# Kernel optimization log

Measured on AMD Instinct MI355X. Metric: run time of the kernel, lower is better.

The kernel has to match this reference:

```python
import jax, jax.numpy as jnp
import numpy as np

TOP_K = 8
NUM_EXPERTS = 64
N_TOKENS = 16384
N_EMBED = 4096
EPS = 1e-12  # F.normalize default eps


def setup_inputs() -> dict:
    key = jax.random.key(0)
    k_x, k_wr, k_br, k_wn, k_bn, k_noise = jax.random.split(key, 6)
    scale = 1.0 / np.sqrt(N_EMBED)
    return {
        "x": jax.random.normal(k_x, (N_TOKENS, N_EMBED), dtype=jnp.float32),
        "w_route": jax.random.normal(k_wr, (N_EMBED, NUM_EXPERTS), dtype=jnp.float32) * scale,
        "b_route": jax.random.normal(k_br, (NUM_EXPERTS,), dtype=jnp.float32) * scale,
        "w_noise": jax.random.normal(k_wn, (N_EMBED, NUM_EXPERTS), dtype=jnp.float32) * scale,
        "b_noise": jax.random.normal(k_bn, (NUM_EXPERTS,), dtype=jnp.float32) * scale,
        "noise": jax.random.normal(k_noise, (N_TOKENS, NUM_EXPERTS), dtype=jnp.float32),
    }


def _l1_normalize(v):
    return v / jnp.maximum(jnp.sum(jnp.abs(v)), EPS)


def reference(x, w_route, b_route, w_noise, b_noise, noise):
    # dual linear projections: [N, D] @ [D, E] -> [N, E]
    logits = x @ w_route + b_route
    noise_logits = x @ w_noise + b_noise
    noisy_logits = logits + noise * jax.nn.softplus(noise_logits)

    # top-k (sorted descending, matches torch.topk)
    top_vals, top_idx = jax.lax.top_k(noisy_logits, TOP_K)  # [N, K]
    rows = jnp.arange(noisy_logits.shape[0])[:, None]

    # scatter top-k logits into -inf, softmax -> sparse gate distribution
    sparse_logits = jnp.full_like(noisy_logits, -jnp.inf).at[rows, top_idx].set(top_vals)
    router_output = jax.nn.softmax(sparse_logits, axis=-1)  # [N, E]

    # aux loss (training path). Faithful to torch scatter semantics:
    # gates[n, top_idx[n, j]] = router_output[n, j] (first K columns of src).
    probs = jax.nn.softmax(noisy_logits, axis=-1)
    gates = jnp.zeros_like(probs).at[rows, top_idx].set(router_output[:, :TOP_K])
    probs_sum = probs.sum(0)                                  # [E]
    freq = (gates > 0).astype(jnp.float32).sum(0)             # [E]
    lsesq = jnp.sum(jax.nn.logsumexp(noisy_logits, axis=-1) ** 2)
    switchloss = NUM_EXPERTS * jnp.sum(_l1_normalize(probs_sum) * _l1_normalize(freq))
    zloss = lsesq / noisy_logits.shape[0]
    aux_loss = switchloss + 0.1 * zloss

    return router_output, top_idx, aux_loss
```

## Files before the change

kernel.cpp:

```cpp
#include <hip/hip_runtime.h>
#include <math.h>

#define NT 16384
#define NE 4096
#define NX 64
#define TK 8

#define BM 32
#define NBLK (NT / BM)
#define NSTEP 64

#define RO_SIZE (NT * NX)
#define TI_OFF  RO_SIZE
#define AUX_IDX (RO_SIZE + NT * TK)

#define MAXFLAG 8192
#define PSB_IDX 8256
#define FRB_IDX (PSB_IDX + NBLK * 64)
#define L2B_IDX (FRB_IDX + NBLK * 64)
#define WS_FLOATS (L2B_IDX + NBLK)
#define BPACK_OFF (((WS_FLOATS * 4) + 255) & ~255)
#define BPACK_USHORTS (128 * 4 * 2 * 128 * 8)
#define WS_NEED ((size_t)BPACK_OFF + (size_t)BPACK_USHORTS * 2)

#define DELTA_FP32 5e-5f
#define DELTA_BF16 2.5e-4f

typedef __attribute__((ext_vector_type(8))) short bf16x8_t;
typedef __attribute__((ext_vector_type(4))) float f32x4_t;

__device__ __forceinline__ float neginf() { return __int_as_float(0xff800000); }

__device__ __forceinline__ unsigned short bf16_trunc(float f) {
    return (unsigned short)(__float_as_uint(f) >> 16);
}
__device__ __forceinline__ unsigned short bf16_rtn(float f) {
    unsigned u = __float_as_uint(f);
    unsigned r = u + 0x7fffu + ((u >> 16) & 1u);
    return (unsigned short)(r >> 16);
}
__device__ __forceinline__ float bf16_to_f(unsigned short h) {
    return __uint_as_float(((unsigned)h) << 16);
}

__device__ __forceinline__ void split4(const float4& f,
                                       unsigned& h0, unsigned& h1,
                                       unsigned& l0, unsigned& l1) {
    unsigned u0 = __float_as_uint(f.x), u1 = __float_as_uint(f.y);
    unsigned u2 = __float_as_uint(f.z), u3 = __float_as_uint(f.w);
    h0 = __builtin_amdgcn_perm(u1, u0, 0x07060302u);
    h1 = __builtin_amdgcn_perm(u3, u2, 0x07060302u);
    float g0 = f.x - __uint_as_float(u0 & 0xffff0000u);
    float g1 = f.y - __uint_as_float(u1 & 0xffff0000u);
    float g2 = f.z - __uint_as_float(u2 & 0xffff0000u);
    float g3 = f.w - __uint_as_float(u3 & 0xffff0000u);
    l0 = __builtin_amdgcn_perm(__float_as_uint(g1), __float_as_uint(g0), 0x07060302u);
    l1 = __builtin_amdgcn_perm(__float_as_uint(g3), __float_as_uint(g2), 0x07060302u);
}

#define GLOAD16(GP, LP) __builtin_amdgcn_global_load_lds(                     \
    (const __attribute__((address_space(1))) void*)(GP),                      \
    (__attribute__((address_space(3))) void*)(LP), 16, 0, 0)

__global__ __launch_bounds__(512) void prep_w_kernel(
    const float* __restrict__ w_route, const float* __restrict__ w_noise,
    unsigned short* __restrict__ bp)
{
    const int kt = blockIdx.x;
    const int t = threadIdx.x;
    const int col = t & 127;
    const int kq = t >> 7;
    const float* src = (col < NX) ? (w_route + col) : (w_noise + (col - NX));
    const int kbase = kt * 32 + kq * 8;
    bf16x8_t h8, l8;
    #pragma unroll
    for (int i = 0; i < 8; ++i) {
        float v = src[(size_t)(kbase + i) * NX];
        unsigned short hh = bf16_trunc(v);
        h8[i] = (short)hh;
        l8[i] = (short)bf16_rtn(v - bf16_to_f(hh));
    }
    unsigned short* base = bp + ((size_t)((kt * 4 + kq) * 2) * 128 + col) * 8;
    *(bf16x8_t*)base = h8;
    *(bf16x8_t*)(base + 128 * 8) = l8;
}

__global__ __launch_bounds__(512, 4) void fused32_kernel(
    const float* __restrict__ x,
    const unsigned short* __restrict__ bp,
    const float* __restrict__ b_route, const float* __restrict__ b_noise,
    const float* __restrict__ noise,
    float* __restrict__ out,
    float* __restrict__ ps_blk, float* __restrict__ fr_blk,
    float* __restrict__ lse2_blk,
    int* __restrict__ flag_cnt, int* __restrict__ flag_list)
{
    __shared__ __align__(16) char ldsraw[81920];

    const int tid = threadIdx.x;
    const int wid = tid >> 6;
    const int lane = tid & 63;
    const int l15 = lane & 15;
    const int kq = lane >> 4;
    const int rg = wid >> 2;
    const int cgq = wid & 3;
    const int bm = blockIdx.x * BM;

    const int srow = tid >> 4;
    const int sq = tid & 15;
    const int skc = sq >> 1;
    const int shalf = sq & 1;
    const int srl = srow & 15;
    const int offA = srow * 256 + ((skc ^ srl) << 4) + shalf * 8;
    const float* sxa = x + (size_t)(bm + srow) * NE + sq * 4;

    char* ldsB = ldsraw + 16384;
    char* dB = ldsB + tid * 16;

    #define STAGE_B(BUF, ST) do {                                             \
        const unsigned short* sB_ = bp + (size_t)(ST) * 16384 + tid * 8;      \
        char* dB_ = dB + (BUF) * 32768;                                       \
        GLOAD16(sB_,         dB_);                                            \
        GLOAD16(sB_ + 4096,  dB_ + 8192);                                     \
        GLOAD16(sB_ + 8192,  dB_ + 16384);                                    \
        GLOAD16(sB_ + 12288, dB_ + 24576);                                    \
    } while (0)

    #define WRITE_A(BUF) do {                                                 \
        unsigned h0_, h1_, l0_, l1_;                                          \
        split4(rx, h0_, h1_, l0_, l1_);                                       \
        const int ob_ = (BUF) * 8192;                                         \
        *(int2*)(ldsraw + ob_ + offA)         = make_int2((int)h0_, (int)h1_);\
        *(int2*)(ldsraw + ob_ + (offA ^ 128)) = make_int2((int)l0_, (int)l1_);\
    } while (0)

    f32x4_t acc0 = (f32x4_t){0.f, 0.f, 0.f, 0.f};
    f32x4_t acc1 = (f32x4_t){0.f, 0.f, 0.f, 0.f};

    float4 rx = *(const float4*)(sxa);
    STAGE_B(0, 0);
    WRITE_A(0);
    __syncthreads();

    const char* aRow = ldsraw + (rg * 16 + l15) * 256;
    const int rl = l15;
    const int bBase = kq * 4096 + (cgq * 32 + l15) * 16;
    const int bLo   = bBase + 2048;

    for (int st = 0; st < NSTEP; ++st) {
        const int cur = st & 1;
        if (st + 1 < NSTEP) {
            rx = *(const float4*)(sxa + (st + 1) * 64);
            STAGE_B(cur ^ 1, st + 1);
        }

        const char* aB = aRow + cur * 8192;
        const char* bT = ldsB + cur * 32768;
        #pragma unroll
        for (int sub = 0; sub < 2; ++sub) {
            const int kcr = sub * 4 + kq;
            const int ch = (kcr ^ rl) << 4;
            bf16x8_t ah = *(const bf16x8_t*)(aB + ch);
            bf16x8_t al = *(const bf16x8_t*)(aB + (ch ^ 128));
            const char* bS = bT + sub * 16384;
            bf16x8_t bh0 = *(const bf16x8_t*)(bS + bBase);
            bf16x8_t bh1 = *(const bf16x8_t*)(bS + bBase + 256);
            bf16x8_t bl0 = *(const bf16x8_t*)(bS + bLo);
            bf16x8_t bl1 = *(const bf16x8_t*)(bS + bLo + 256);
            acc0 = __builtin_amdgcn_mfma_f32_16x16x32_bf16(ah, bh0, acc0, 0, 0, 0);
            acc1 = __builtin_amdgcn_mfma_f32_16x16x32_bf16(ah, bh1, acc1, 0, 0, 0);
            acc0 = __builtin_amdgcn_mfma_f32_16x16x32_bf16(al, bh0, acc0, 0, 0, 0);
            acc1 = __builtin_amdgcn_mfma_f32_16x16x32_bf16(al, bh1, acc1, 0, 0, 0);
            acc0 = __builtin_amdgcn_mfma_f32_16x16x32_bf16(ah, bl0, acc0, 0, 0, 0);
            acc1 = __builtin_amdgcn_mfma_f32_16x16x32_bf16(ah, bl1, acc1, 0, 0, 0);
        }

        if (st + 1 < NSTEP) WRITE_A(cur ^ 1);
        __syncthreads();
    }
    #undef STAGE_B
    #undef WRITE_A

    float (*part)[130] = (float (*)[130])ldsraw;
    #pragma unroll
    for (int j = 0; j < 4; ++j) {
        int tok = rg * 16 + (lane >> 4) * 4 + j;
        part[tok][cgq * 32 + l15]      = acc0[j];
        part[tok][cgq * 32 + 16 + l15] = acc1[j];
    }
    __syncthreads();

    const float br = b_route[lane];
    const float bnv = b_noise[lane];
    float ps_l = 0.f, fr_l = 0.f, l2_l = 0.f;

    for (int tt = 0; tt < 4; ++tt) {
        const int tok = wid * 4 + tt;
        const int gt  = bm + tok;
        float lr = part[tok][lane] + br;
        float ln = part[tok][64 + lane] + bnv;
        float nz = noise[(size_t)gt * NX + lane];
        float sp = fmaxf(ln, 0.f) + log1pf(expf(-fabsf(ln)));
        float v  = lr + nz * sp;

        float vv = v;
        float tv[9]; int ti[9];
        #pragma unroll
        for (int s = 0; s < 9; ++s) {
            float mv = vv; int mi = lane;
            #pragma unroll
            for (int off = 32; off > 0; off >>= 1) {
                float ov = __shfl_xor(mv, off);
                int   oi = __shfl_xor(mi, off);
                if (ov > mv || (ov == mv && oi < mi)) { mv = ov; mi = oi; }
            }
            tv[s] = mv; ti[s] = mi;
            if (lane == mi) vv = neginf();
        }

        float ming = 1e30f;
        #pragma unroll
        for (int s = 0; s < 8; ++s) ming = fminf(ming, tv[s] - tv[s + 1]);
        if (lane == 0 && ming < DELTA_BF16) {
            int p = atomicAdd(flag_cnt, 1);
            if (p < MAXFLAG) flag_list[p] = gt;
        }

        const float m0 = tv[0];
        float e8[8], s8 = 0.f;
        #pragma unroll
        for (int s = 0; s < 8; ++s) { e8[s] = expf(tv[s] - m0); s8 += e8[s]; }
        float r = 0.f;
        #pragma unroll
        for (int s = 0; s < 8; ++s) if (ti[s] == lane) r = e8[s] / s8;
        out[(size_t)gt * NX + lane] = r;
        if (lane < TK) out[TI_OFF + (size_t)gt * TK + lane] = (float)ti[lane];

        float p = expf(v - m0);
        float s64 = p;
        #pragma unroll
        for (int off = 32; off > 0; off >>= 1) s64 += __shfl_xor(s64, off);
        ps_l += p / s64;
        if (lane == 0) { float lse = m0 + logf(s64); l2_l += lse * lse; }

        unsigned tm8 = 0;
        #pragma unroll
        for (int s = 0; s < 8; ++s) if (ti[s] < TK) tm8 |= (1u << ti[s]);
        #pragma unroll
        for (int s = 0; s < 8; ++s)
            if (ti[s] == lane && ((tm8 >> s) & 1u)) fr_l += 1.f;
    }

    float* sps = (float*)(ldsraw + 20480);
    float* sfr = (float*)(ldsraw + 20480 + 2048);
    float* sl2 = (float*)(ldsraw + 20480 + 4096);
    sps[wid * 64 + lane] = ps_l;
    sfr[wid * 64 + lane] = fr_l;
    if (lane == 0) sl2[wid] = l2_l;
    __syncthreads();
    if (wid == 0) {
        float a = 0.f, b = 0.f;
        #pragma unroll
        for (int w = 0; w < 8; ++w) {
            a += sps[w * 64 + lane];
            b += sfr[w * 64 + lane];
        }
        ps_blk[(size_t)blockIdx.x * 64 + lane] = a;
        fr_blk[(size_t)blockIdx.x * 64 + lane] = b;
        if (lane == 0) {
            float z = 0.f;
            #pragma unroll
            for (int w = 0; w < 8; ++w) z += sl2[w];
            lse2_blk[blockIdx.x] = z;
        }
    }
}

#define FBM 64
#define FBN 128
#define FBK 32
#define XPITCH (FBM + 4)
__global__ __launch_bounds__(256) void fused_router_kernel(
    const float* __restrict__ x,
    const float* __restrict__ w_route, const float* __restrict__ b_route,
    const float* __restrict__ w_noise, const float* __restrict__ b_noise,
    const float* __restrict__ noise,
    float* __restrict__ out,
    float* __restrict__ ps_acc, float* __restrict__ fr_acc,
    float* __restrict__ lse2_acc,
    int* __restrict__ flag_cnt, int* __restrict__ flag_list)
{
    __shared__ float smem[FBM * FBN];
    float* xs  = smem;
    float* wst = smem + FBK * XPITCH;
    const int tid = threadIdx.x;
    const int block_m = blockIdx.x * FBM;
    const int row0 = (tid >> 5) * 8;
    const int col0 = (tid & 31) * 4;
    float acc[8][4];
    #pragma unroll
    for (int i = 0; i < 8; ++i)
        #pragma unroll
        for (int j = 0; j < 4; ++j) acc[i][j] = 0.f;
    float4 px[2], pw[4];
    {
        #pragma unroll
        for (int s = 0; s < 2; ++s) {
            int f = tid + s * 256, r = f >> 3, kqv = f & 7;
            px[s] = *reinterpret_cast<const float4*>(x + (size_t)(block_m + r) * NE + kqv * 4);
        }
        #pragma unroll
        for (int s = 0; s < 4; ++s) {
            int f = tid + s * 256, kk = f >> 5, c4 = (f & 31) * 4;
            const float* src = (c4 < NX) ? (w_route + (size_t)kk * NX + c4)
                                         : (w_noise + (size_t)kk * NX + (c4 - NX));
            pw[s] = *reinterpret_cast<const float4*>(src);
        }
    }
    for (int t = 0; t < NE / FBK; ++t) {
        __syncthreads();
        #pragma unroll
        for (int s = 0; s < 2; ++s) {
            int f = tid + s * 256, r = f >> 3, kqv = f & 7;
            xs[(kqv * 4 + 0) * XPITCH + r] = px[s].x;
            xs[(kqv * 4 + 1) * XPITCH + r] = px[s].y;
            xs[(kqv * 4 + 2) * XPITCH + r] = px[s].z;
            xs[(kqv * 4 + 3) * XPITCH + r] = px[s].w;
        }
        #pragma unroll
        for (int s = 0; s < 4; ++s) {
            int f = tid + s * 256, kk = f >> 5, c4 = (f & 31) * 4;
            *reinterpret_cast<float4*>(&wst[kk * FBN + c4]) = pw[s];
        }
        __syncthreads();
        if (t + 1 < NE / FBK) {
            const int k0 = (t + 1) * FBK;
            #pragma unroll
            for (int s = 0; s < 2; ++s) {
                int f = tid + s * 256, r = f >> 3, kqv = f & 7;
                px[s] = *reinterpret_cast<const float4*>(x + (size_t)(block_m + r) * NE + k0 + kqv * 4);
            }
            #pragma unroll
            for (int s = 0; s < 4; ++s) {
                int f = tid + s * 256, kk = f >> 5, c4 = (f & 31) * 4;
                const float* src = (c4 < NX) ? (w_route + (size_t)(k0 + kk) * NX + c4)
                                             : (w_noise + (size_t)(k0 + kk) * NX + (c4 - NX));
                pw[s] = *reinterpret_cast<const float4*>(src);
            }
        }
        #pragma unroll
        for (int k = 0; k < FBK; ++k) {
            float4 xa = *reinterpret_cast<const float4*>(&xs[k * XPITCH + row0]);
            float4 xb = *reinterpret_cast<const float4*>(&xs[k * XPITCH + row0 + 4]);
            float4 wv = *reinterpret_cast<const float4*>(&wst[k * FBN + col0]);
            float xf[8] = {xa.x, xa.y, xa.z, xa.w, xb.x, xb.y, xb.z, xb.w};
            float wf[4] = {wv.x, wv.y, wv.z, wv.w};
            #pragma unroll
            for (int i = 0; i < 8; ++i)
                #pragma unroll
                for (int j = 0; j < 4; ++j)
                    acc[i][j] = fmaf(xf[i], wf[j], acc[i][j]);
        }
    }
    __syncthreads();
    #pragma unroll
    for (int i = 0; i < 8; ++i) {
        float4 v = make_float4(acc[i][0], acc[i][1], acc[i][2], acc[i][3]);
        *reinterpret_cast<float4*>(&smem[(row0 + i) * FBN + col0]) = v;
    }
    __syncthreads();
    const int wave = tid >> 6;
    const int lane = tid & 63;
    const float br = b_route[lane];
    const float bnv = b_noise[lane];
    float ps_l = 0.f, fr_l = 0.f, l2_l = 0.f;
    for (int tt = 0; tt < FBM / 4; ++tt) {
        const int tok = wave * (FBM / 4) + tt;
        const int gt  = block_m + tok;
        float lr = smem[tok * FBN + lane] + br;
        float ln = smem[tok * FBN + NX + lane] + bnv;
        float nz = noise[(size_t)gt * NX + lane];
        float sp = fmaxf(ln, 0.f) + log1pf(expf(-fabsf(ln)));
        float v  = lr + nz * sp;
        float vv = v;
        float tv[9]; int ti[9];
        #pragma unroll
        for (int s = 0; s < 9; ++s) {
            float mv = vv; int mi = lane;
            #pragma unroll
            for (int off = 32; off > 0; off >>= 1) {
                float ov = __shfl_xor(mv, off);
                int   oi = __shfl_xor(mi, off);
                if (ov > mv || (ov == mv && oi < mi)) { mv = ov; mi = oi; }
            }
            tv[s] = mv; ti[s] = mi;
            if (lane == mi) vv = neginf();
        }
        float ming = 1e30f;
        #pragma unroll
        for (int s = 0; s < 8; ++s) ming = fminf(ming, tv[s] - tv[s + 1]);
        if (lane == 0 && ming < DELTA_FP32) {
            int p = atomicAdd(flag_cnt, 1);
            if (p < MAXFLAG) flag_list[p] = gt;
        }
        const float m0 = tv[0];
        float e8[8], s8 = 0.f;
        #pragma unroll
        for (int s = 0; s < 8; ++s) { e8[s] = expf(tv[s] - m0); s8 += e8[s]; }
        float r = 0.f;
        #pragma unroll
        for (int s = 0; s < 8; ++s) if (ti[s] == lane) r = e8[s] / s8;
        out[(size_t)gt * NX + lane] = r;
        if (lane < TK) out[TI_OFF + (size_t)gt * TK + lane] = (float)ti[lane];
        float p = expf(v - m0);
        float s64 = p;
        #pragma unroll
        for (int off = 32; off > 0; off >>= 1) s64 += __shfl_xor(s64, off);
        ps_l += p / s64;
        if (lane == 0) { float lse = m0 + logf(s64); l2_l += lse * lse; }
        unsigned tm8 = 0;
        #pragma unroll
        for (int s = 0; s < 8; ++s) if (ti[s] < TK) tm8 |= (1u << ti[s]);
        #pragma unroll
        for (int s = 0; s < 8; ++s)
            if (ti[s] == lane && ((tm8 >> s) & 1u)) fr_l += 1.f;
    }
    atomicAdd(&ps_acc[lane], ps_l);
    atomicAdd(&fr_acc[lane], fr_l);
    if (lane == 0) atomicAdd(lse2_acc, l2_l);
}

__global__ __launch_bounds__(256) void refine_kernel(
    const float* __restrict__ x, const float* __restrict__ w_route,
    const float* __restrict__ b_route, const float* __restrict__ w_noise,
    const float* __restrict__ b_noise, const float* __restrict__ noise,
    float* __restrict__ out, const int* __restrict__ flag_cnt,
    const int* __restrict__ flag_list)
{
    __shared__ double red[8][64];
    const int tid = threadIdx.x;
    const int lane = tid & 63, wq = tid >> 6;
    int nf = *flag_cnt; if (nf > MAXFLAG) nf = MAXFLAG;
    for (int fi = blockIdx.x; fi < nf; fi += gridDim.x) {
        const int gt = flag_list[fi];
        const float* xr = x + (size_t)gt * NE + wq * 1024;
        const float* wr = w_route + (size_t)wq * 1024 * NX;
        const float* wn = w_noise + (size_t)wq * 1024 * NX;
        double ar0 = 0, ar1 = 0, an0 = 0, an1 = 0;
        for (int k = 0; k < 1024; k += 2) {
            double x0 = xr[k], x1 = xr[k + 1];
            ar0 += x0 * (double)wr[(size_t)k * NX + lane];
            ar1 += x1 * (double)wr[(size_t)(k + 1) * NX + lane];
            an0 += x0 * (double)wn[(size_t)k * NX + lane];
            an1 += x1 * (double)wn[(size_t)(k + 1) * NX + lane];
        }
        red[wq * 2][lane]     = ar0 + ar1;
        red[wq * 2 + 1][lane] = an0 + an1;
        __syncthreads();
        if (tid < 64) {
            double lr = red[0][lane] + red[2][lane] + red[4][lane] + red[6][lane]
                      + (double)b_route[lane];
            double ln = red[1][lane] + red[3][lane] + red[5][lane] + red[7][lane]
                      + (double)b_noise[lane];
            double nz = (double)noise[(size_t)gt * NX + lane];
            double sp = (ln > 0.0) ? (ln + log1p(exp(-ln))) : log1p(exp(ln));
            double v  = lr + nz * sp;
            double vv = v;
            double tv[8]; int ti[8];
            #pragma unroll
            for (int s = 0; s < 8; ++s) {
                double mv = vv; int mi = lane;
                #pragma unroll
                for (int off = 32; off > 0; off >>= 1) {
                    double ov = __shfl_xor(mv, off);
                    int    oi = __shfl_xor(mi, off);
                    if (ov > mv || (ov == mv && oi < mi)) { mv = ov; mi = oi; }
                }
                tv[s] = mv; ti[s] = mi;
                if (lane == mi) vv = -1.0e300;
            }
            double m0 = tv[0], s8 = 0.0, e8[8];
            #pragma unroll
            for (int s = 0; s < 8; ++s) { e8[s] = exp(tv[s] - m0); s8 += e8[s]; }
            float r = 0.f;
            #pragma unroll
            for (int s = 0; s < 8; ++s) if (ti[s] == lane) r = (float)(e8[s] / s8);
            out[(size_t)gt * NX + lane] = r;
            if (lane < TK) out[TI_OFF + (size_t)gt * TK + lane] = (float)ti[lane];
        }
        __syncthreads();
    }
}

__global__ __launch_bounds__(512) void finalize_kernel(
    const float* __restrict__ ps_blk, const float* __restrict__ fr_blk,
    const float* __restrict__ lse2_blk, float* __restrict__ out)
{
    __shared__ float sps[8][64], sfr[8][64], sl2[512];
    const int t = threadIdx.x;
    const int e = t & 63, g = t >> 6;
    float a = 0.f, b = 0.f;
    for (int blk = g; blk < NBLK; blk += 8) {
        a += ps_blk[(size_t)blk * 64 + e];
        b += fr_blk[(size_t)blk * 64 + e];
    }
    sps[g][e] = a;
    sfr[g][e] = b;
    sl2[t] = lse2_blk[t];
    __syncthreads();
    if (t < 64) {
        float p = 0.f, f = 0.f;
        #pragma unroll
        for (int gg = 0; gg < 8; ++gg) { p += sps[gg][t]; f += sfr[gg][t]; }
        float z = 0.f;
        #pragma unroll
        for (int i = 0; i < 8; ++i) z += sl2[t * 8 + i];
        float sp = p, sf = f, sz = z;
        #pragma unroll
        for (int off = 32; off > 0; off >>= 1) {
            sp += __shfl_xor(sp, off);
            sf += __shfl_xor(sf, off);
            sz += __shfl_xor(sz, off);
        }
        float d = (p / fmaxf(sp, 1e-12f)) * (f / fmaxf(sf, 1e-12f));
        #pragma unroll
        for (int off = 32; off > 0; off >>= 1) d += __shfl_xor(d, off);
        if (t == 0)
            out[AUX_IDX] = 64.f * d + 0.1f * (sz / (float)NT);
    }
}

extern "C" void kernel_launch(void* const* d_in, const int* in_sizes, int n_in,
                              void* d_out, int out_size, void* d_ws, size_t ws_size,
                              hipStream_t stream) {
    const float* x       = (const float*)d_in[0];
    const float* w_route = (const float*)d_in[1];
    const float* b_route = (const float*)d_in[2];
    const float* w_noise = (const float*)d_in[3];
    const float* b_noise = (const float*)d_in[4];
    const float* noise   = (const float*)d_in[5];
    float* out = (float*)d_out;

    float* wsf = (float*)d_ws;
    int* flag_cnt  = (int*)wsf;
    int* flag_list = (int*)(wsf + 1);
    float* ps_blk   = wsf + PSB_IDX;
    float* fr_blk   = wsf + FRB_IDX;
    float* lse2_blk = wsf + L2B_IDX;

    hipMemsetAsync(d_ws, 0, (size_t)(1 + MAXFLAG) * sizeof(int), stream);

    if (ws_size >= WS_NEED) {
        unsigned short* bpack = (unsigned short*)((char*)d_ws + BPACK_OFF);
        prep_w_kernel<<<128, 512, 0, stream>>>(w_route, w_noise, bpack);
        fused32_kernel<<<NBLK, 512, 0, stream>>>(
            x, bpack, b_route, b_noise, noise, out,
            ps_blk, fr_blk, lse2_blk, flag_cnt, flag_list);
    } else {
        hipMemsetAsync(ps_blk, 0,
                       (size_t)(WS_FLOATS - PSB_IDX) * sizeof(float), stream);
        fused_router_kernel<<<NT / FBM, 256, 0, stream>>>(
            x, w_route, b_route, w_noise, b_noise, noise, out,
            ps_blk, fr_blk, lse2_blk, flag_cnt, flag_list);
    }

    refine_kernel<<<1024, 256, 0, stream>>>(
        x, w_route, b_route, w_noise, b_noise, noise, out, flag_cnt, flag_list);

    finalize_kernel<<<1, 512, 0, stream>>>(ps_blk, fr_blk, lse2_blk, out);
}
```

Measured before the change: 199.5 us.

## Switch GEMM to 32x32x16 MFMA with split-K across waves and unrolled double buffer

Replaces the 16x16x32 MFMA tiling, where each wave covered 16 rows by 32 columns, with 32x32x16 MFMA. Each wave now covers all 32 rows by 32 columns for half of the K chunk, and the two K-halves are reduced through LDS in the epilogue. The main loop is unrolled by two with fixed buffer indices and separate prefetch registers. The aim is fewer LDS fragment loads per MFMA and less loop overhead, at the cost of a larger LDS partial buffer, an extra reduction add, and 16 accumulator registers per lane.

```diff
diff --git a/kernel.cpp b/kernel.cpp
--- a/kernel.cpp
+++ b/kernel.cpp
@@ -28,6 +28,7 @@
 
 typedef __attribute__((ext_vector_type(8))) short bf16x8_t;
 typedef __attribute__((ext_vector_type(4))) float f32x4_t;
+typedef __attribute__((ext_vector_type(16))) float f32x16_t;
 
 __device__ __forceinline__ float neginf() { return __int_as_float(0xff800000); }
 
@@ -100,10 +101,10 @@
     const int tid = threadIdx.x;
     const int wid = tid >> 6;
     const int lane = tid & 63;
-    const int l15 = lane & 15;
-    const int kq = lane >> 4;
-    const int rg = wid >> 2;
+    const int l31 = lane & 31;
+    const int lhi = lane >> 5;
     const int cgq = wid & 3;
+    const int kh = wid >> 2;
     const int bm = blockIdx.x * BM;
 
     const int srow = tid >> 4;
@@ -126,67 +127,69 @@
         GLOAD16(sB_ + 12288, dB_ + 24576);                                    \
     } while (0)
 
-    #define WRITE_A(BUF) do {                                                 \
+    #define WRITE_A(BUF, RX) do {                                             \
         unsigned h0_, h1_, l0_, l1_;                                          \
-        split4(rx, h0_, h1_, l0_, l1_);                                       \
+        split4(RX, h0_, h1_, l0_, l1_);                                       \
         const int ob_ = (BUF) * 8192;                                         \
         *(int2*)(ldsraw + ob_ + offA)         = make_int2((int)h0_, (int)h1_);\
         *(int2*)(ldsraw + ob_ + (offA ^ 128)) = make_int2((int)l0_, (int)l1_);\
     } while (0)
 
-    f32x4_t acc0 = (f32x4_t){0.f, 0.f, 0.f, 0.f};
-    f32x4_t acc1 = (f32x4_t){0.f, 0.f, 0.f, 0.f};
-
-    float4 rx = *(const float4*)(sxa);
+    f32x16_t acc;
+    #pragma unroll
+    for (int i = 0; i < 16; ++i) acc[i] = 0.f;
+
+    const int r15 = l31 & 15;
+    const int adrA0 = l31 * 256 + (((4 * kh + 0 + lhi) ^ r15) << 4);
+    const int adrA1 = l31 * 256 + (((4 * kh + 2 + lhi) ^ r15) << 4);
+    const int offB = kh * 16384 + lhi * 4096 + (cgq * 32 + l31) * 16;
+
+    #define COMPUTE(CUR) do {                                                 \
+        const char* aB_ = ldsraw + (CUR) * 8192;                              \
+        const char* bT_ = ldsB + (CUR) * 32768;                               \
+        bf16x8_t ah0 = *(const bf16x8_t*)(aB_ + adrA0);                       \
+        bf16x8_t al0 = *(const bf16x8_t*)(aB_ + (adrA0 ^ 128));               \
+        bf16x8_t bh0 = *(const bf16x8_t*)(bT_ + offB);                        \
+        bf16x8_t bl0 = *(const bf16x8_t*)(bT_ + offB + 2048);                 \
+        acc = __builtin_amdgcn_mfma_f32_32x32x16_bf16(ah0, bh0, acc, 0, 0, 0);\
+        acc = __builtin_amdgcn_mfma_f32_32x32x16_bf16(al0, bh0, acc, 0, 0, 0);\
+        acc = __builtin_amdgcn_mfma_f32_32x32x16_bf16(ah0, bl0, acc, 0, 0, 0);\
+        bf16x8_t ah1 = *(const bf16x8_t*)(aB_ + adrA1);                       \
+        bf16x8_t al1 = *(const bf16x8_t*)(aB_ + (adrA1 ^ 128));               \
+        bf16x8_t bh1 = *(const bf16x8_t*)(bT_ + offB + 8192);                 \
+        bf16x8_t bl1 = *(const bf16x8_t*)(bT_ + offB + 8192 + 2048);          \
+        acc = __builtin_amdgcn_mfma_f32_32x32x16_bf16(ah1, bh1, acc, 0, 0, 0);\
+        acc = __builtin_amdgcn_mfma_f32_32x32x16_bf16(al1, bh1, acc, 0, 0, 0);\
+        acc = __builtin_amdgcn_mfma_f32_32x32x16_bf16(ah1, bl1, acc, 0, 0, 0);\
+    } while (0)
+
+    float4 rxA = *(const float4*)(sxa);
     STAGE_B(0, 0);
-    WRITE_A(0);
+    WRITE_A(0, rxA);
+    float4 rxB = *(const float4*)(sxa + 64);
     __syncthreads();
 
-    const char* aRow = ldsraw + (rg * 16 + l15) * 256;
-    const int rl = l15;
-    const int bBase = kq * 4096 + (cgq * 32 + l15) * 16;
-    const int bLo   = bBase + 2048;
-
-    for (int st = 0; st < NSTEP; ++st) {
-        const int cur = st & 1;
-        if (st + 1 < NSTEP) {
-            rx = *(const float4*)(sxa + (st + 1) * 64);
-            STAGE_B(cur ^ 1, st + 1);
-        }
-
-        const char* aB = aRow + cur * 8192;
-        const char* bT = ldsB + cur * 32768;
-        #pragma unroll
-        for (int sub = 0; sub < 2; ++sub) {
-            const int kcr = sub * 4 + kq;
-            const int ch = (kcr ^ rl) << 4;
-            bf16x8_t ah = *(const bf16x8_t*)(aB + ch);
-            bf16x8_t al = *(const bf16x8_t*)(aB + (ch ^ 128));
-            const char* bS = bT + sub * 16384;
-            bf16x8_t bh0 = *(const bf16x8_t*)(bS + bBase);
-            bf16x8_t bh1 = *(const bf16x8_t*)(bS + bBase + 256);
-            bf16x8_t bl0 = *(const bf16x8_t*)(bS + bLo);
-            bf16x8_t bl1 = *(const bf16x8_t*)(bS + bLo + 256);
-            acc0 = __builtin_amdgcn_mfma_f32_16x16x32_bf16(ah, bh0, acc0, 0, 0, 0);
-            acc1 = __builtin_amdgcn_mfma_f32_16x16x32_bf16(ah, bh1, acc1, 0, 0, 0);
-            acc0 = __builtin_amdgcn_mfma_f32_16x16x32_bf16(al, bh0, acc0, 0, 0, 0);
-            acc1 = __builtin_amdgcn_mfma_f32_16x16x32_bf16(al, bh1, acc1, 0, 0, 0);
-            acc0 = __builtin_amdgcn_mfma_f32_16x16x32_bf16(ah, bl0, acc0, 0, 0, 0);
-            acc1 = __builtin_amdgcn_mfma_f32_16x16x32_bf16(ah, bl1, acc1, 0, 0, 0);
-        }
-
-        if (st + 1 < NSTEP) WRITE_A(cur ^ 1);
+    for (int t = 0; t < NSTEP; t += 2) {
+        if (t + 2 < NSTEP) rxA = *(const float4*)(sxa + (t + 2) * 64);
+        if (t + 1 < NSTEP) STAGE_B(1, t + 1);
+        COMPUTE(0);
+        if (t + 1 < NSTEP) WRITE_A(1, rxB);
+        __syncthreads();
+        if (t + 3 < NSTEP) rxB = *(const float4*)(sxa + (t + 3) * 64);
+        if (t + 2 < NSTEP) STAGE_B(0, t + 2);
+        COMPUTE(1);
+        if (t + 2 < NSTEP) WRITE_A(0, rxA);
         __syncthreads();
     }
     #undef STAGE_B
     #undef WRITE_A
-
-    float (*part)[130] = (float (*)[130])ldsraw;
+    #undef COMPUTE
+
+    float (*part)[32][132] = (float (*)[32][132])ldsraw;
     #pragma unroll
-    for (int j = 0; j < 4; ++j) {
-        int tok = rg * 16 + (lane >> 4) * 4 + j;
-        part[tok][cgq * 32 + l15]      = acc0[j];
-        part[tok][cgq * 32 + 16 + l15] = acc1[j];
+    for (int r = 0; r < 16; ++r) {
+        int row = (r & 3) + 8 * (r >> 2) + 4 * lhi;
+        part[kh][row][cgq * 32 + l31] = acc[r];
     }
     __syncthreads();
 
@@ -197,8 +200,8 @@
     for (int tt = 0; tt < 4; ++tt) {
         const int tok = wid * 4 + tt;
         const int gt  = bm + tok;
-        float lr = part[tok][lane] + br;
-        float ln = part[tok][64 + lane] + bnv;
+        float lr = part[0][tok][lane] + part[1][tok][lane] + br;
+        float ln = part[0][tok][64 + lane] + part[1][tok][64 + lane] + bnv;
         float nz = noise[(size_t)gt * NX + lane];
         float sp = fmaxf(ln, 0.f) + log1pf(expf(-fabsf(ln)));
         float v  = lr + nz * sp;
@@ -251,9 +254,9 @@
             if (ti[s] == lane && ((tm8 >> s) & 1u)) fr_l += 1.f;
     }
 
-    float* sps = (float*)(ldsraw + 20480);
-    float* sfr = (float*)(ldsraw + 20480 + 2048);
-    float* sl2 = (float*)(ldsraw + 20480 + 4096);
+    float* sps = (float*)(ldsraw + 34816);
+    float* sfr = (float*)(ldsraw + 34816 + 2048);
+    float* sl2 = (float*)(ldsraw + 34816 + 4096);
     sps[wid * 64 + lane] = ps_l;
     sfr[wid * 64 + lane] = fr_l;
     if (lane == 0) sl2[wid] = l2_l;
```

Result: faster. 193.8 us (-2.8%).
